# Optimization experiments

Measured on AMD Instinct MI355X. Metric: run time of the kernel, lower is better.

The kernel has to match this reference:

```python
import jax, jax.numpy as jnp
import numpy as np

THRESHOLD = 1.0


def heaviside(x):
    return (x > 0).astype(x.dtype)


def lif_parallel(x, W_ih, b_ih, b_hh, beta):
    """snntorch LeakyParallel: RNN with relu nonlinearity and diagonal
    recurrent weight = beta, followed by threshold spike (no reset).
    x: [T, B, I]; W_ih: [H, I]; beta: [H]. Returns spikes [T, B, H]."""
    beta = jnp.clip(beta, 0.0, 1.0)
    # input projection is time-parallel (one big GEMM)
    z = jnp.einsum('tbi,hi->tbh', x, W_ih) + b_ih + b_hh  # [T, B, H]

    def step(h, z_t):
        h_new = jax.nn.relu(z_t + beta * h)
        return h_new, h_new

    h0 = jnp.zeros(z.shape[1:], z.dtype)
    _, mem = jax.lax.scan(step, h0, z)  # [T, B, H]
    return heaviside(mem - THRESHOLD)


def setup_inputs() -> dict:
    key = jax.random.key(0)
    ks = jax.random.split(key, 9)
    T, B, I, H, O = 200, 256, 784, 1000, 10
    s1 = 1.0 / np.sqrt(I)
    s2 = 1.0 / np.sqrt(H)
    return {
        'x': jax.random.normal(ks[0], (T, B, I), dtype=jnp.float32),
        'W_ih1': jax.random.normal(ks[1], (H, I), dtype=jnp.float32) * s1,
        'b_ih1': jax.random.normal(ks[2], (H,), dtype=jnp.float32) * s1,
        'b_hh1': jax.random.normal(ks[3], (H,), dtype=jnp.float32) * s1,
        'beta1': jnp.full((H,), 0.95, dtype=jnp.float32),
        'W_ih2': jax.random.normal(ks[4], (O, H), dtype=jnp.float32) * s2,
        'b_ih2': jax.random.normal(ks[5], (O,), dtype=jnp.float32) * s2,
        'b_hh2': jax.random.normal(ks[6], (O,), dtype=jnp.float32) * s2,
        'beta2': jnp.full((O,), 0.95, dtype=jnp.float32),
    }


def reference(x, W_ih1, b_ih1, b_hh1, beta1, W_ih2, b_ih2, b_hh2, beta2):
    spk1 = lif_parallel(x, W_ih1, b_ih1, b_hh1, beta1)   # [T, B, 1000]
    spk2 = lif_parallel(spk1, W_ih2, b_ih2, b_hh2, beta2)  # [T, B, 10]
    return spk2
```

## Files before the change

### kernel.cpp

```cpp
#include <hip/hip_runtime.h>
#include <cstdint>
#include <cstddef>

#define T_STEPS 200
#define B_SZ    256
#define I_SZ    784
#define H_SZ    1000
#define O_SZ    10
#define M_ROWS  (T_STEPS * B_SZ)

#define BM 64
#define BN 64
#define BK 32

__global__ __launch_bounds__(256) void gemm1_kernel(
    const float* __restrict__ X, const float* __restrict__ W,
    const float* __restrict__ b_ih, const float* __restrict__ b_hh,
    float* __restrict__ Z)
{
    __shared__ float As[BK][BM + 4];
    __shared__ float Bs[BK][BN + 4];

    const int tid  = threadIdx.x;
    const int row0 = blockIdx.x * BM;
    const int col0 = blockIdx.y * BN;
    const int tr   = tid >> 4;
    const int tc   = tid & 15;

    float acc[4][4] = {};

    for (int k0 = 0; k0 < I_SZ; k0 += BK) {
        #pragma unroll
        for (int l = 0; l < 2; ++l) {
            int id = tid + l * 256;
            int r  = id >> 3;
            int c4 = id & 7;
            int k  = k0 + c4 * 4;

            float4 av = make_float4(0.f, 0.f, 0.f, 0.f);
            if (k + 4 <= I_SZ)
                av = *(const float4*)(X + (size_t)(row0 + r) * I_SZ + k);
            As[c4*4+0][r] = av.x; As[c4*4+1][r] = av.y;
            As[c4*4+2][r] = av.z; As[c4*4+3][r] = av.w;

            float4 bv = make_float4(0.f, 0.f, 0.f, 0.f);
            int n = col0 + r;
            if (n < H_SZ && k + 4 <= I_SZ)
                bv = *(const float4*)(W + (size_t)n * I_SZ + k);
            Bs[c4*4+0][r] = bv.x; Bs[c4*4+1][r] = bv.y;
            Bs[c4*4+2][r] = bv.z; Bs[c4*4+3][r] = bv.w;
        }
        __syncthreads();

        #pragma unroll
        for (int k = 0; k < BK; ++k) {
            float a[4], b[4];
            #pragma unroll
            for (int i = 0; i < 4; ++i) a[i] = As[k][tr*4 + i];
            #pragma unroll
            for (int j = 0; j < 4; ++j) b[j] = Bs[k][tc*4 + j];
            #pragma unroll
            for (int i = 0; i < 4; ++i)
                #pragma unroll
                for (int j = 0; j < 4; ++j)
                    acc[i][j] = fmaf(a[i], b[j], acc[i][j]);
        }
        __syncthreads();
    }

    #pragma unroll
    for (int i = 0; i < 4; ++i) {
        int rr = row0 + tr*4 + i;
        #pragma unroll
        for (int j = 0; j < 4; ++j) {
            int cc = col0 + tc*4 + j;
            if (cc < H_SZ)
                Z[(size_t)rr * H_SZ + cc] = acc[i][j] + b_ih[cc] + b_hh[cc];
        }
    }
}

__global__ __launch_bounds__(256) void scan1_kernel(
    float* __restrict__ Z, const float* __restrict__ beta)
{
    int idx = blockIdx.x * blockDim.x + threadIdx.x;
    if (idx >= B_SZ * H_SZ) return;
    int h = idx % H_SZ;
    float be = fminf(fmaxf(beta[h], 0.f), 1.f);
    float hm = 0.f;
    const size_t stride = (size_t)B_SZ * H_SZ;
    float* p = Z + idx;
    for (int t = 0; t < T_STEPS; ++t) {
        float v = p[(size_t)t * stride];
        hm = fmaxf(fmaf(be, hm, v), 0.f);
        p[(size_t)t * stride] = (hm > 1.0f) ? 1.0f : 0.0f;
    }
}

__global__ __launch_bounds__(256) void gemm2_kernel(
    const float* __restrict__ S, const float* __restrict__ W2,
    const float* __restrict__ b_ih2, const float* __restrict__ b_hh2,
    float* __restrict__ Z2)
{
    __shared__ float W2s[O_SZ * H_SZ];
    for (int i = threadIdx.x; i < O_SZ * H_SZ; i += blockDim.x)
        W2s[i] = W2[i];
    __syncthreads();

    const int wave  = threadIdx.x >> 6;
    const int lane  = threadIdx.x & 63;
    const int wgid  = blockIdx.x * (blockDim.x >> 6) + wave;
    const int nwave = gridDim.x * (blockDim.x >> 6);

    for (int m = wgid; m < M_ROWS; m += nwave) {
        const float* row = S + (size_t)m * H_SZ;
        float acc[O_SZ];
        #pragma unroll
        for (int o = 0; o < O_SZ; ++o) acc[o] = 0.f;

        for (int h = lane; h < H_SZ; h += 64) {
            float s = row[h];
            #pragma unroll
            for (int o = 0; o < O_SZ; ++o)
                acc[o] = fmaf(s, W2s[o * H_SZ + h], acc[o]);
        }
        #pragma unroll
        for (int o = 0; o < O_SZ; ++o) {
            float v = acc[o];
            #pragma unroll
            for (int off = 32; off > 0; off >>= 1)
                v += __shfl_down(v, off, 64);
            if (lane == 0)
                Z2[(size_t)m * O_SZ + o] = v + b_ih2[o] + b_hh2[o];
        }
    }
}

#define CH 20
__global__ __launch_bounds__(256) void scan2_kernel(
    const float* __restrict__ Z2, const float* __restrict__ beta2,
    float* __restrict__ out)
{
    int idx = blockIdx.x * blockDim.x + threadIdx.x;
    if (idx >= B_SZ * O_SZ) return;
    int o = idx % O_SZ;
    float be = fminf(fmaxf(beta2[o], 0.f), 1.f);
    float hm = 0.f;
    const int stride = B_SZ * O_SZ;
    for (int t0 = 0; t0 < T_STEPS; t0 += CH) {
        float v[CH];
        #pragma unroll
        for (int i = 0; i < CH; ++i)
            v[i] = Z2[(size_t)(t0 + i) * stride + idx];
        #pragma unroll
        for (int i = 0; i < CH; ++i) {
            hm = fmaxf(fmaf(be, hm, v[i]), 0.f);
            out[(size_t)(t0 + i) * stride + idx] = (hm > 1.0f) ? 1.0f : 0.0f;
        }
    }
}

extern "C" void kernel_launch(void* const* d_in, const int* in_sizes, int n_in,
                              void* d_out, int out_size, void* d_ws, size_t ws_size,
                              hipStream_t stream)
{
    const float* x     = (const float*)d_in[0];
    const float* W1    = (const float*)d_in[1];
    const float* bih1  = (const float*)d_in[2];
    const float* bhh1  = (const float*)d_in[3];
    const float* beta1 = (const float*)d_in[4];
    const float* W2    = (const float*)d_in[5];
    const float* bih2  = (const float*)d_in[6];
    const float* bhh2  = (const float*)d_in[7];
    const float* beta2 = (const float*)d_in[8];
    float* out = (float*)d_out;

    float* z1 = (float*)d_ws;
    float* z2 = z1 + (size_t)M_ROWS * H_SZ;

    dim3 g1(M_ROWS / BM, (H_SZ + BN - 1) / BN);
    gemm1_kernel<<<g1, 256, 0, stream>>>(x, W1, bih1, bhh1, z1);

    scan1_kernel<<<(B_SZ * H_SZ) / 256, 256, 0, stream>>>(z1, beta1);

    gemm2_kernel<<<2048, 256, 0, stream>>>(z1, W2, bih2, bhh2, z2);

    scan2_kernel<<<(B_SZ * O_SZ + 255) / 256, 256, 0, stream>>>(z2, beta2, out);
}
```

Baseline: 1.334 ms.

## Enlarge GEMM1 tiles to 128x128 with 8x8 register blocking and swizzled LDS

Rewrites the input-projection GEMM with 128x128 block tiles and an 8x8 per-thread micro-tile, so each thread does more FMAs per shared-memory read. Shared-memory layout uses a swizzle plus padding so the float4 reads avoid bank conflicts. Output stores are vectorised as float4 with a hoisted bias. The cost is a larger register footprint (64 accumulators) that may limit occupancy, and more edge-tile waste on the 1000-wide N dimension.

After: 1.203 ms. -9.8%, faster.

```diff
diff --git a/kernel.cpp b/kernel.cpp
--- a/kernel.cpp
+++ b/kernel.cpp
@@ -9,73 +9,109 @@
 #define O_SZ    10
 #define M_ROWS  (T_STEPS * B_SZ)
 
-#define BM 64
-#define BN 64
-#define BK 32
-
-__global__ __launch_bounds__(256) void gemm1_kernel(
+#define GBM 128
+#define GBN 128
+#define GBK 32
+#define LDW 132
+
+__device__ __forceinline__ int swz(int g) {
+    return (g & 24) | ((g + (g >> 3)) & 7);
+}
+
+__global__ __launch_bounds__(256, 4) void gemm1_fp32_v2(
     const float* __restrict__ X, const float* __restrict__ W,
     const float* __restrict__ b_ih, const float* __restrict__ b_hh,
     float* __restrict__ Z)
 {
-    __shared__ float As[BK][BM + 4];
-    __shared__ float Bs[BK][BN + 4];
+    __shared__ float As[GBK * LDW];
+    __shared__ float Bs[GBK * LDW];
 
     const int tid  = threadIdx.x;
-    const int row0 = blockIdx.x * BM;
-    const int col0 = blockIdx.y * BN;
     const int tr   = tid >> 4;
     const int tc   = tid & 15;
-
-    float acc[4][4] = {};
-
-    for (int k0 = 0; k0 < I_SZ; k0 += BK) {
-        #pragma unroll
-        for (int l = 0; l < 2; ++l) {
+    const int row0 = blockIdx.x * GBM;
+    const int col0 = blockIdx.y * GBN;
+
+    const int a0 = swz(2 * tr)     * 4;
+    const int a1 = swz(2 * tr + 1) * 4;
+    const int b0 = swz(2 * tc)     * 4;
+    const int b1 = swz(2 * tc + 1) * 4;
+
+    float acc[8][8] = {};
+
+    const float* Xp = X + (size_t)row0 * I_SZ;
+    const float* Wp = W + (size_t)col0 * I_SZ;
+
+    for (int k0 = 0; k0 < I_SZ; k0 += GBK) {
+        #pragma unroll
+        for (int l = 0; l < 4; ++l) {
             int id = tid + l * 256;
             int r  = id >> 3;
             int c4 = id & 7;
             int k  = k0 + c4 * 4;
+            int base = swz(r >> 2) * 4 + (r & 3);
 
             float4 av = make_float4(0.f, 0.f, 0.f, 0.f);
             if (k + 4 <= I_SZ)
-                av = *(const float4*)(X + (size_t)(row0 + r) * I_SZ + k);
-            As[c4*4+0][r] = av.x; As[c4*4+1][r] = av.y;
-            As[c4*4+2][r] = av.z; As[c4*4+3][r] = av.w;
+                av = *(const float4*)(Xp + (size_t)r * I_SZ + k);
+            As[(4*c4 + 0) * LDW + base] = av.x;
+            As[(4*c4 + 1) * LDW + base] = av.y;
+            As[(4*c4 + 2) * LDW + base] = av.z;
+            As[(4*c4 + 3) * LDW + base] = av.w;
 
             float4 bv = make_float4(0.f, 0.f, 0.f, 0.f);
-            int n = col0 + r;
-            if (n < H_SZ && k + 4 <= I_SZ)
-                bv = *(const float4*)(W + (size_t)n * I_SZ + k);
-            Bs[c4*4+0][r] = bv.x; Bs[c4*4+1][r] = bv.y;
-            Bs[c4*4+2][r] = bv.z; Bs[c4*4+3][r] = bv.w;
+            if (k + 4 <= I_SZ && col0 + r < H_SZ)
+                bv = *(const float4*)(Wp + (size_t)r * I_SZ + k);
+            Bs[(4*c4 + 0) * LDW + base] = bv.x;
+            Bs[(4*c4 + 1) * LDW + base] = bv.y;
+            Bs[(4*c4 + 2) * LDW + base] = bv.z;
+            Bs[(4*c4 + 3) * LDW + base] = bv.w;
         }
         __syncthreads();
 
-        #pragma unroll
-        for (int k = 0; k < BK; ++k) {
-            float a[4], b[4];
-            #pragma unroll
-            for (int i = 0; i < 4; ++i) a[i] = As[k][tr*4 + i];
-            #pragma unroll
-            for (int j = 0; j < 4; ++j) b[j] = Bs[k][tc*4 + j];
-            #pragma unroll
-            for (int i = 0; i < 4; ++i)
+        #pragma unroll 4
+        for (int k = 0; k < GBK; ++k) {
+            const int kb = k * LDW;
+            float4 A0 = *(const float4*)&As[kb + a0];
+            float4 A1 = *(const float4*)&As[kb + a1];
+            float4 B0 = *(const float4*)&Bs[kb + b0];
+            float4 B1 = *(const float4*)&Bs[kb + b1];
+            float a[8] = {A0.x, A0.y, A0.z, A0.w, A1.x, A1.y, A1.z, A1.w};
+            float b[8] = {B0.x, B0.y, B0.z, B0.w, B1.x, B1.y, B1.z, B1.w};
+            #pragma unroll
+            for (int i = 0; i < 8; ++i)
                 #pragma unroll
-                for (int j = 0; j < 4; ++j)
+                for (int j = 0; j < 8; ++j)
                     acc[i][j] = fmaf(a[i], b[j], acc[i][j]);
         }
         __syncthreads();
     }
 
+    float bias[8];
     #pragma unroll
-    for (int i = 0; i < 4; ++i) {
-        int rr = row0 + tr*4 + i;
-        #pragma unroll
-        for (int j = 0; j < 4; ++j) {
-            int cc = col0 + tc*4 + j;
-            if (cc < H_SZ)
-                Z[(size_t)rr * H_SZ + cc] = acc[i][j] + b_ih[cc] + b_hh[cc];
+    for (int j = 0; j < 8; ++j) {
+        int cc = col0 + tc * 8 + j;
+        bias[j] = (cc < H_SZ) ? (b_ih[cc] + b_hh[cc]) : 0.f;
+    }
+
+    const bool full = (col0 + 127 < H_SZ);
+    #pragma unroll
+    for (int i = 0; i < 8; ++i) {
+        int rr = row0 + tr * 8 + i;
+        float* zrow = Z + (size_t)rr * H_SZ + col0 + tc * 8;
+        if (full) {
+            float4 v0 = make_float4(acc[i][0] + bias[0], acc[i][1] + bias[1],
+                                    acc[i][2] + bias[2], acc[i][3] + bias[3]);
+            float4 v1 = make_float4(acc[i][4] + bias[4], acc[i][5] + bias[5],
+                                    acc[i][6] + bias[6], acc[i][7] + bias[7]);
+            *(float4*)(zrow + 0) = v0;
+            *(float4*)(zrow + 4) = v1;
+        } else {
+            #pragma unroll
+            for (int j = 0; j < 8; ++j) {
+                int cc = col0 + tc * 8 + j;
+                if (cc < H_SZ) zrow[j] = acc[i][j] + bias[j];
+            }
         }
     }
 }
@@ -178,12 +214,10 @@
     float* z1 = (float*)d_ws;
     float* z2 = z1 + (size_t)M_ROWS * H_SZ;
 
-    dim3 g1(M_ROWS / BM, (H_SZ + BN - 1) / BN);
-    gemm1_kernel<<<g1, 256, 0, stream>>>(x, W1, bih1, bhh1, z1);
+    dim3 g1(M_ROWS / GBM, (H_SZ + GBN - 1) / GBN);
+    gemm1_fp32_v2<<<g1, 256, 0, stream>>>(x, W1, bih1, bhh1, z1);
 
     scan1_kernel<<<(B_SZ * H_SZ) / 256, 256, 0, stream>>>(z1, beta1);
-
     gemm2_kernel<<<2048, 256, 0, stream>>>(z1, W2, bih2, bhh2, z2);
-
     scan2_kernel<<<(B_SZ * O_SZ + 255) / 256, 256, 0, stream>>>(z2, beta2, out);
 }
```
